# Kernel optimization log

Hardware: AMD Instinct MI355X
Metric: run time of the kernel (lower is better)

Reference implementation:

```python
import jax, jax.numpy as jnp
import numpy as np

U, I, D, E, L = 100000, 50000, 64, 600000, 3
N = U + I  # total nodes in bipartite graph


def setup_inputs() -> dict:
    key = jax.random.key(0)
    k1, k2, k3, k4 = jax.random.split(key, 4)
    user_emb = jax.random.normal(k1, (U, D), dtype=jnp.float32) * 0.1
    item_emb = jax.random.normal(k2, (I, D), dtype=jnp.float32) * 0.1
    # random user-item interactions; symmetrize to build the (U+I)x(U+I) adjacency
    u = jax.random.randint(k3, (E,), 0, U)
    i = jax.random.randint(k4, (E,), 0, I) + U
    edge_src = jnp.concatenate([u, i])  # [2E]
    edge_dst = jnp.concatenate([i, u])  # [2E]
    # symmetric normalization: A_hat[s,d] = 1/sqrt(deg_s * deg_d)
    deg = jax.ops.segment_sum(jnp.ones((2 * E,), jnp.float32), edge_dst, num_segments=N)
    dinv = jnp.where(deg > 0, 1.0 / jnp.sqrt(deg), 0.0)
    edge_vals = dinv[edge_src] * dinv[edge_dst]
    return {
        "user_emb": user_emb,
        "item_emb": item_emb,
        "edge_src": edge_src,
        "edge_dst": edge_dst,
        "edge_vals": edge_vals,
    }


def reference(user_emb, item_emb, edge_src, edge_dst, edge_vals):
    # LightGCN propagation: ego_{k+1} = A_hat @ ego_k, then mean over the L layer outputs
    ego = jnp.concatenate([user_emb, item_emb], axis=0)  # [N, D]
    acc = jnp.zeros_like(ego)
    for _ in range(L):  # fixed small layer count
        msgs = edge_vals[:, None] * ego[edge_src]  # [2E, D] gather + scale
        ego = jax.ops.segment_sum(msgs, edge_dst, num_segments=N)  # SpMM via scatter-add
        acc = acc + ego
    mean_emb = acc / L
    return mean_emb[:U], mean_emb[U:]
```

## Files before the change

### kernel.cpp

```cpp
#include <hip/hip_runtime.h>

#define U_CNT 100000
#define I_CNT 50000
#define D_DIM 64
#define N_NODES 150000
#define SCAN_BLK 256

__device__ __forceinline__ float blo(unsigned u) { return __uint_as_float(u << 16); }
__device__ __forceinline__ float bhi(unsigned u) { return __uint_as_float(u & 0xFFFF0000u); }
__device__ __forceinline__ unsigned f2b(float f) {
    unsigned b = __float_as_uint(f);
    return (b + 0x7FFFu + ((b >> 16) & 1u)) >> 16;
}
__device__ __forceinline__ unsigned pack2(float a, float b) {
    return f2b(a) | (f2b(b) << 16);
}


__global__ void deg_hist_rank(const int* __restrict__ dst, int* __restrict__ deg,
                              int* __restrict__ rank, int nE) {
    int e = blockIdx.x * blockDim.x + threadIdx.x;
    if (e < nE) rank[e] = atomicAdd(&deg[dst[e]], 1);
}

__global__ void block_sums(const int* __restrict__ deg, int* __restrict__ blksum, int n) {
    __shared__ int sm[SCAN_BLK];
    int i = blockIdx.x * SCAN_BLK + threadIdx.x;
    sm[threadIdx.x] = (i < n) ? deg[i] : 0;
    __syncthreads();
    for (int off = SCAN_BLK / 2; off > 0; off >>= 1) {
        if (threadIdx.x < off) sm[threadIdx.x] += sm[threadIdx.x + off];
        __syncthreads();
    }
    if (threadIdx.x == 0) blksum[blockIdx.x] = sm[0];
}

__global__ void scan_blksums(const int* __restrict__ blksum, int* __restrict__ blkoff,
                             int* __restrict__ row_ptr, int nb) {
    __shared__ int sm[1024];
    int t = threadIdx.x;
    int v = (t < nb) ? blksum[t] : 0;
    sm[t] = v;
    __syncthreads();
    for (int off = 1; off < 1024; off <<= 1) {
        int x = (t >= off) ? sm[t - off] : 0;
        __syncthreads();
        sm[t] += x;
        __syncthreads();
    }
    if (t < nb) blkoff[t] = sm[t] - v;
    if (t == nb - 1) row_ptr[N_NODES] = sm[t];
}

__global__ void scan_within(const int* __restrict__ deg, const int* __restrict__ blkoff,
                            int* __restrict__ row_ptr, int n) {
    __shared__ int sm[SCAN_BLK];
    int i = blockIdx.x * SCAN_BLK + threadIdx.x;
    int t = threadIdx.x;
    int d = (i < n) ? deg[i] : 0;
    sm[t] = d;
    __syncthreads();
    for (int off = 1; off < SCAN_BLK; off <<= 1) {
        int x = (t >= off) ? sm[t - off] : 0;
        __syncthreads();
        sm[t] += x;
        __syncthreads();
    }
    if (i < n) row_ptr[i] = blkoff[blockIdx.x] + sm[t] - d;
}

__global__ void csr_fill(const int* __restrict__ src, const int* __restrict__ dst,
                         const float* __restrict__ val, const int* __restrict__ row_ptr,
                         const int* __restrict__ rank, int2* __restrict__ csr, int nE) {
    int e = blockIdx.x * blockDim.x + threadIdx.x;
    if (e < 4) csr[nE + e] = make_int2(0, 0);
    if (e >= nE) return;
    int pos = row_ptr[dst[e]] + rank[e];
    csr[pos] = make_int2(src[e], __float_as_int(val[e]));
}

__global__ void to_bf16(const float4* __restrict__ user4, const float4* __restrict__ item4,
                        uint2* __restrict__ ego0, int n4u, int n4) {
    int i = blockIdx.x * blockDim.x + threadIdx.x;
    if (i >= n4) return;
    float4 f = (i < n4u) ? user4[i] : item4[i - n4u];
    ego0[i] = make_uint2(pack2(f.x, f.y), pack2(f.z, f.w));
}

__device__ __forceinline__ void fma8(float (&acc)[8], float v, uint4 g) {
    acc[0] = fmaf(v, blo(g.x), acc[0]); acc[1] = fmaf(v, bhi(g.x), acc[1]);
    acc[2] = fmaf(v, blo(g.y), acc[2]); acc[3] = fmaf(v, bhi(g.y), acc[3]);
    acc[4] = fmaf(v, blo(g.z), acc[4]); acc[5] = fmaf(v, bhi(g.z), acc[5]);
    acc[6] = fmaf(v, blo(g.w), acc[6]); acc[7] = fmaf(v, bhi(g.w), acc[7]);
}

template <int FINAL>
__global__ void lgcn_spmm(const int* __restrict__ row_ptr,
                          const int2* __restrict__ csr,
                          const uint4* __restrict__ ego_in,
                          uint4* __restrict__ ego_out,
                          const uint4* __restrict__ egoA,
                          const uint4* __restrict__ egoB,
                          float4* __restrict__ out) {
    int node = (blockIdx.x * blockDim.x + threadIdx.x) >> 3;
    int l    = threadIdx.x & 7;
    if (node >= N_NODES) return;
    int beg = row_ptr[node];
    int end = row_ptr[node + 1];

    float a0[8] = {0, 0, 0, 0, 0, 0, 0, 0};
    float a1[8] = {0, 0, 0, 0, 0, 0, 0, 0};

    int2 e0 = csr[beg], e1 = csr[beg + 1], e2 = csr[beg + 2], e3 = csr[beg + 3];
    int j = beg;
    while (j + 4 <= end) {
        uint4 x0 = ego_in[(size_t)e0.x * 8 + l];
        uint4 x1 = ego_in[(size_t)e1.x * 8 + l];
        uint4 x2 = ego_in[(size_t)e2.x * 8 + l];
        uint4 x3 = ego_in[(size_t)e3.x * 8 + l];
        int2 n0 = csr[j + 4], n1 = csr[j + 5], n2 = csr[j + 6], n3 = csr[j + 7];
        fma8(a0, __int_as_float(e0.y), x0);
        fma8(a1, __int_as_float(e1.y), x1);
        fma8(a0, __int_as_float(e2.y), x2);
        fma8(a1, __int_as_float(e3.y), x3);
        e0 = n0; e1 = n1; e2 = n2; e3 = n3;
        j += 4;
    }
    int rem = end - j;
    if (rem > 0) fma8(a0, __int_as_float(e0.y), ego_in[(size_t)e0.x * 8 + l]);
    if (rem > 1) fma8(a1, __int_as_float(e1.y), ego_in[(size_t)e1.x * 8 + l]);
    if (rem > 2) fma8(a0, __int_as_float(e2.y), ego_in[(size_t)e2.x * 8 + l]);

    float acc[8];
#pragma unroll
    for (int k = 0; k < 8; ++k) acc[k] = a0[k] + a1[k];

    if (!FINAL) {
        uint4 r;
        r.x = pack2(acc[0], acc[1]); r.y = pack2(acc[2], acc[3]);
        r.z = pack2(acc[4], acc[5]); r.w = pack2(acc[6], acc[7]);
        ego_out[(size_t)node * 8 + l] = r;
    } else {
        uint4 a = egoA[(size_t)node * 8 + l];
        uint4 b = egoB[(size_t)node * 8 + l];
        const float s = 1.0f / 3.0f;
        float4 o0, o1;
        o0.x = (blo(a.x) + blo(b.x) + acc[0]) * s;
        o0.y = (bhi(a.x) + bhi(b.x) + acc[1]) * s;
        o0.z = (blo(a.y) + blo(b.y) + acc[2]) * s;
        o0.w = (bhi(a.y) + bhi(b.y) + acc[3]) * s;
        o1.x = (blo(a.z) + blo(b.z) + acc[4]) * s;
        o1.y = (bhi(a.z) + bhi(b.z) + acc[5]) * s;
        o1.z = (blo(a.w) + blo(b.w) + acc[6]) * s;
        o1.w = (bhi(a.w) + bhi(b.w) + acc[7]) * s;
        size_t ob = (size_t)node * 16 + 2 * l;
        out[ob]     = o0;
        out[ob + 1] = o1;
    }
}

static inline size_t align_up(size_t x, size_t a) { return (x + a - 1) & ~(a - 1); }

extern "C" void kernel_launch(void* const* d_in, const int* in_sizes, int n_in,
                              void* d_out, int out_size, void* d_ws, size_t ws_size,
                              hipStream_t stream) {
    const float* user_emb  = (const float*)d_in[0];
    const float* item_emb  = (const float*)d_in[1];
    const int*   edge_src  = (const int*)d_in[2];
    const int*   edge_dst  = (const int*)d_in[3];
    const float* edge_vals = (const float*)d_in[4];
    const int    nE        = in_sizes[2];

    float* out = (float*)d_out;
    const size_t nd = (size_t)N_NODES * D_DIM;
    const size_t row_u4 = 8;

    size_t off = 0;
    char* base = (char*)d_ws;
    int2* csr = (int2*)(base + off);      off = align_up(off + (size_t)(nE + 4) * sizeof(int2), 256);
    int* row_ptr = (int*)(base + off);    off = align_up(off + (size_t)(N_NODES + 1) * 4, 256);
    uint4* ego0 = (uint4*)(base + off);   off = align_up(off + (size_t)N_NODES * row_u4 * 16, 256);
    uint4* ego_a = (uint4*)(base + off);  off = align_up(off + (size_t)N_NODES * row_u4 * 16, 256);
    uint4* ego_b = (uint4*)(base + off);  off = align_up(off + (size_t)N_NODES * row_u4 * 16, 256);

    const int NB = (N_NODES + SCAN_BLK - 1) / SCAN_BLK;
    int* rank   = (int*)ego_a;
    int* deg    = rank + nE;
    int* blksum = deg + N_NODES;
    int* blkoff = blksum + NB;

    const int block = 256;

    hipMemsetAsync(deg, 0, (size_t)N_NODES * 4, stream);
    deg_hist_rank<<<(nE + block - 1) / block, block, 0, stream>>>(edge_dst, deg, rank, nE);
    block_sums<<<NB, SCAN_BLK, 0, stream>>>(deg, blksum, N_NODES);
    scan_blksums<<<1, 1024, 0, stream>>>(blksum, blkoff, row_ptr, NB);
    scan_within<<<NB, SCAN_BLK, 0, stream>>>(deg, blkoff, row_ptr, N_NODES);
    csr_fill<<<(nE + block - 1) / block, block, 0, stream>>>(
        edge_src, edge_dst, edge_vals, row_ptr, rank, csr, nE);

    const int n4  = (int)(nd / 4);
    const int n4u = U_CNT * D_DIM / 4;
    to_bf16<<<(n4 + block - 1) / block, block, 0, stream>>>(
        (const float4*)user_emb, (const float4*)item_emb, (uint2*)ego0, n4u, n4);

    const size_t threads = (size_t)N_NODES * 8;
    const int spmm_grid = (int)((threads + block - 1) / block);

    lgcn_spmm<0><<<spmm_grid, block, 0, stream>>>(
        row_ptr, csr, ego0, ego_a, nullptr, nullptr, nullptr);
    lgcn_spmm<0><<<spmm_grid, block, 0, stream>>>(
        row_ptr, csr, ego_a, ego_b, nullptr, nullptr, nullptr);
    lgcn_spmm<1><<<spmm_grid, block, 0, stream>>>(
        row_ptr, csr, ego_b, nullptr, ego_a, ego_b, (float4*)out);
}
```

Measured before the change: 267.4 us.

## Build CSR via two-level bucket sort with shared-memory histograms

Replaces the global-atomic degree histogram and random-scatter CSR fill with a two-pass bucketed counting sort. Edges are first binned by dst>>8 using per-chunk shared-memory histograms and a global scan, then each bucket is sorted locally in LDS to emit CSR rows and row_ptr. The bf16 conversion is folded into the histogram kernel. This aims to cut global atomic contention and uncoalesced scatter writes, at the cost of an extra temporary edge buffer, more kernels, and bucket sizes limited by the shared-memory cache capacity, with a global-memory fallback when a bucket exceeds it.

```diff
diff --git a/kernel.cpp b/kernel.cpp
--- a/kernel.cpp
+++ b/kernel.cpp
@@ -4,7 +4,10 @@
 #define I_CNT 50000
 #define D_DIM 64
 #define N_NODES 150000
-#define SCAN_BLK 256
+#define CHUNK 2048
+#define NBKT 586
+#define SCAN_BLK 512
+#define CCAP 3584
 
 __device__ __forceinline__ float blo(unsigned u) { return __uint_as_float(u << 16); }
 __device__ __forceinline__ float bhi(unsigned u) { return __uint_as_float(u & 0xFFFF0000u); }
@@ -16,17 +19,31 @@
     return f2b(a) | (f2b(b) << 16);
 }
 
-
-__global__ void deg_hist_rank(const int* __restrict__ dst, int* __restrict__ deg,
-                              int* __restrict__ rank, int nE) {
-    int e = blockIdx.x * blockDim.x + threadIdx.x;
-    if (e < nE) rank[e] = atomicAdd(&deg[dst[e]], 1);
-}
-
-__global__ void block_sums(const int* __restrict__ deg, int* __restrict__ blksum, int n) {
+__global__ void bucket_hist(const int* __restrict__ dst, int* __restrict__ H,
+                            int NB_B, int nE,
+                            const float4* __restrict__ user4,
+                            const float4* __restrict__ item4,
+                            uint2* __restrict__ ego0, int n4u, int n4) {
+    __shared__ int h[NBKT];
+    for (int i = threadIdx.x; i < NBKT; i += blockDim.x) h[i] = 0;
+    __syncthreads();
+    int b = blockIdx.x;
+    int beg = b * CHUNK, end = min(nE, beg + CHUNK);
+    for (int e = beg + (int)threadIdx.x; e < end; e += blockDim.x)
+        atomicAdd(&h[dst[e] >> 8], 1);
+    __syncthreads();
+    for (int i = threadIdx.x; i < NBKT; i += blockDim.x) H[i * NB_B + b] = h[i];
+    int gsz = gridDim.x * blockDim.x;
+    for (int i = blockIdx.x * blockDim.x + threadIdx.x; i < n4; i += gsz) {
+        float4 f = (i < n4u) ? user4[i] : item4[i - n4u];
+        ego0[i] = make_uint2(pack2(f.x, f.y), pack2(f.z, f.w));
+    }
+}
+
+__global__ void block_sums(const int* __restrict__ in, int* __restrict__ blksum, int n) {
     __shared__ int sm[SCAN_BLK];
     int i = blockIdx.x * SCAN_BLK + threadIdx.x;
-    sm[threadIdx.x] = (i < n) ? deg[i] : 0;
+    sm[threadIdx.x] = (i < n) ? in[i] : 0;
     __syncthreads();
     for (int off = SCAN_BLK / 2; off > 0; off >>= 1) {
         if (threadIdx.x < off) sm[threadIdx.x] += sm[threadIdx.x + off];
@@ -35,8 +52,7 @@
     if (threadIdx.x == 0) blksum[blockIdx.x] = sm[0];
 }
 
-__global__ void scan_blksums(const int* __restrict__ blksum, int* __restrict__ blkoff,
-                             int* __restrict__ row_ptr, int nb) {
+__global__ void scan_blksums(const int* __restrict__ blksum, int* __restrict__ blkoff, int nb) {
     __shared__ int sm[1024];
     int t = threadIdx.x;
     int v = (t < nb) ? blksum[t] : 0;
@@ -49,15 +65,13 @@
         __syncthreads();
     }
     if (t < nb) blkoff[t] = sm[t] - v;
-    if (t == nb - 1) row_ptr[N_NODES] = sm[t];
-}
-
-__global__ void scan_within(const int* __restrict__ deg, const int* __restrict__ blkoff,
-                            int* __restrict__ row_ptr, int n) {
+}
+
+__global__ void scan_within(int* __restrict__ H, const int* __restrict__ blkoff, int n) {
     __shared__ int sm[SCAN_BLK];
     int i = blockIdx.x * SCAN_BLK + threadIdx.x;
     int t = threadIdx.x;
-    int d = (i < n) ? deg[i] : 0;
+    int d = (i < n) ? H[i] : 0;
     sm[t] = d;
     __syncthreads();
     for (int off = 1; off < SCAN_BLK; off <<= 1) {
@@ -66,25 +80,71 @@
         sm[t] += x;
         __syncthreads();
     }
-    if (i < n) row_ptr[i] = blkoff[blockIdx.x] + sm[t] - d;
-}
-
-__global__ void csr_fill(const int* __restrict__ src, const int* __restrict__ dst,
-                         const float* __restrict__ val, const int* __restrict__ row_ptr,
-                         const int* __restrict__ rank, int2* __restrict__ csr, int nE) {
-    int e = blockIdx.x * blockDim.x + threadIdx.x;
-    if (e < 4) csr[nE + e] = make_int2(0, 0);
-    if (e >= nE) return;
-    int pos = row_ptr[dst[e]] + rank[e];
-    csr[pos] = make_int2(src[e], __float_as_int(val[e]));
-}
-
-__global__ void to_bf16(const float4* __restrict__ user4, const float4* __restrict__ item4,
-                        uint2* __restrict__ ego0, int n4u, int n4) {
-    int i = blockIdx.x * blockDim.x + threadIdx.x;
-    if (i >= n4) return;
-    float4 f = (i < n4u) ? user4[i] : item4[i - n4u];
-    ego0[i] = make_uint2(pack2(f.x, f.y), pack2(f.z, f.w));
+    if (i < n) H[i] = blkoff[blockIdx.x] + sm[t] - d;
+}
+
+__global__ void bucket_scatter(const int* __restrict__ src, const int* __restrict__ dst,
+                               const float* __restrict__ val, const int* __restrict__ Hs,
+                               uint2* __restrict__ tmp, int NB_B, int nE) {
+    __shared__ int cur[NBKT];
+    int b = blockIdx.x;
+    for (int i = threadIdx.x; i < NBKT; i += blockDim.x) cur[i] = Hs[i * NB_B + b];
+    __syncthreads();
+    int beg = b * CHUNK, end = min(nE, beg + CHUNK);
+    for (int e = beg + (int)threadIdx.x; e < end; e += blockDim.x) {
+        int d = dst[e];
+        int pos = atomicAdd(&cur[d >> 8], 1);
+        tmp[pos] = make_uint2((unsigned)src[e] | ((unsigned)(d & 255) << 18),
+                              __float_as_uint(val[e]));
+    }
+}
+
+__global__ void bucket_build(const int* __restrict__ Hs, const uint2* __restrict__ tmp,
+                             int2* __restrict__ csr, int* __restrict__ row_ptr,
+                             int NB_B, int nE) {
+    __shared__ int hist[256];
+    __shared__ int scanbuf[256];
+    __shared__ int cur[256];
+    __shared__ uint2 cache[CCAP];
+    int bkt  = blockIdx.x;
+    int base = Hs[(size_t)bkt * NB_B];
+    int endp = (bkt + 1 < NBKT) ? Hs[(size_t)(bkt + 1) * NB_B] : nE;
+    int size = endp - base;
+    int nbins = min(256, N_NODES - bkt * 256);
+    int t = threadIdx.x;
+
+    hist[t] = 0;
+    __syncthreads();
+    bool cached = (size <= CCAP);
+    for (int k = t; k < size; k += blockDim.x) {
+        uint2 r = tmp[base + k];
+        if (cached) cache[k] = r;
+        atomicAdd(&hist[(r.x >> 18) & 255], 1);
+    }
+    __syncthreads();
+    int v = hist[t];
+    scanbuf[t] = v;
+    __syncthreads();
+    for (int off = 1; off < 256; off <<= 1) {
+        int x = (t >= off) ? scanbuf[t - off] : 0;
+        __syncthreads();
+        scanbuf[t] += x;
+        __syncthreads();
+    }
+    int ex = scanbuf[t] - v;
+    if (t < nbins) row_ptr[bkt * 256 + t] = base + ex;
+    cur[t] = ex;
+    __syncthreads();
+    if (bkt == NBKT - 1) {
+        if (t == 0) row_ptr[N_NODES] = nE;
+        if (t < 4)  csr[nE + t] = make_int2(0, 0);
+    }
+    for (int k = t; k < size; k += blockDim.x) {
+        uint2 r = cached ? cache[k] : tmp[base + k];
+        int f = (r.x >> 18) & 255;
+        int p = atomicAdd(&cur[f], 1);
+        csr[base + p] = make_int2((int)(r.x & 0x3FFFFu), (int)r.y);
+    }
 }
 
 __device__ __forceinline__ void fma8(float (&acc)[8], float v, uint4 g) {
@@ -173,36 +233,34 @@
 
     float* out = (float*)d_out;
     const size_t nd = (size_t)N_NODES * D_DIM;
-    const size_t row_u4 = 8;
+
+    const int NB_B = (nE + CHUNK - 1) / CHUNK;
+    const int nH   = NBKT * NB_B;
+    const int NBs  = (nH + SCAN_BLK - 1) / SCAN_BLK;
 
     size_t off = 0;
     char* base = (char*)d_ws;
-    int2* csr = (int2*)(base + off);      off = align_up(off + (size_t)(nE + 4) * sizeof(int2), 256);
-    int* row_ptr = (int*)(base + off);    off = align_up(off + (size_t)(N_NODES + 1) * 4, 256);
-    uint4* ego0 = (uint4*)(base + off);   off = align_up(off + (size_t)N_NODES * row_u4 * 16, 256);
-    uint4* ego_a = (uint4*)(base + off);  off = align_up(off + (size_t)N_NODES * row_u4 * 16, 256);
-    uint4* ego_b = (uint4*)(base + off);  off = align_up(off + (size_t)N_NODES * row_u4 * 16, 256);
-
-    const int NB = (N_NODES + SCAN_BLK - 1) / SCAN_BLK;
-    int* rank   = (int*)ego_a;
-    int* deg    = rank + nE;
-    int* blksum = deg + N_NODES;
-    int* blkoff = blksum + NB;
+    int2*  csr     = (int2*)(base + off);  off = align_up(off + (size_t)(nE + 4) * sizeof(int2), 256);
+    int*   row_ptr = (int*)(base + off);   off = align_up(off + (size_t)(N_NODES + 1) * 4, 256);
+    uint2* tmp     = (uint2*)(base + off); off = align_up(off + (size_t)nE * sizeof(uint2), 256);
+    int*   H       = (int*)(base + off);   off = align_up(off + (size_t)nH * 4, 256);
+    int*   blksum  = (int*)(base + off);   off = align_up(off + (size_t)NBs * 4, 256);
+    int*   blkoff  = (int*)(base + off);   off = align_up(off + (size_t)NBs * 4, 256);
+    uint4* ego0    = (uint4*)(base + off); off = align_up(off + (size_t)N_NODES * 128, 256);
+    uint4* ego_a   = (uint4*)(base + off); off = align_up(off + (size_t)N_NODES * 128, 256);
+    uint4* ego_b   = (uint4*)(base + off); off = align_up(off + (size_t)N_NODES * 128, 256);
 
     const int block = 256;
-
-    hipMemsetAsync(deg, 0, (size_t)N_NODES * 4, stream);
-    deg_hist_rank<<<(nE + block - 1) / block, block, 0, stream>>>(edge_dst, deg, rank, nE);
-    block_sums<<<NB, SCAN_BLK, 0, stream>>>(deg, blksum, N_NODES);
-    scan_blksums<<<1, 1024, 0, stream>>>(blksum, blkoff, row_ptr, NB);
-    scan_within<<<NB, SCAN_BLK, 0, stream>>>(deg, blkoff, row_ptr, N_NODES);
-    csr_fill<<<(nE + block - 1) / block, block, 0, stream>>>(
-        edge_src, edge_dst, edge_vals, row_ptr, rank, csr, nE);
-
     const int n4  = (int)(nd / 4);
     const int n4u = U_CNT * D_DIM / 4;
-    to_bf16<<<(n4 + block - 1) / block, block, 0, stream>>>(
+
+    bucket_hist<<<NB_B, block, 0, stream>>>(edge_dst, H, NB_B, nE,
         (const float4*)user_emb, (const float4*)item_emb, (uint2*)ego0, n4u, n4);
+    block_sums<<<NBs, SCAN_BLK, 0, stream>>>(H, blksum, nH);
+    scan_blksums<<<1, 1024, 0, stream>>>(blksum, blkoff, NBs);
+    scan_within<<<NBs, SCAN_BLK, 0, stream>>>(H, blkoff, nH);
+    bucket_scatter<<<NB_B, block, 0, stream>>>(edge_src, edge_dst, edge_vals, H, tmp, NB_B, nE);
+    bucket_build<<<NBKT, block, 0, stream>>>(H, tmp, csr, row_ptr, NB_B, nE);
 
     const size_t threads = (size_t)N_NODES * 8;
     const int spmm_grid = (int)((threads + block - 1) / block);
```

Result: faster. 235.9 us (-11.8%).
